# Optimization experiments

Hardware: AMD Instinct MI355X
Metric: run time of the kernel (lower is better)

## Reference

```python
import jax, jax.numpy as jnp
import numpy as np

HID = 1024
N_HEADS = 16
HEAD_DIM = HID // N_HEADS  # 64
SCALE = float(np.sqrt(HEAD_DIM))  # 8.0
# dba_l1 constants from the source
SCALING = float(np.sqrt(0.72676)) * SCALE
CENTER = SCALE ** 2 * 1.12838


def setup_inputs() -> dict:
    key = jax.random.key(0)
    kq, kk, kv = jax.random.split(key, 3)
    B, LQ, LK = 4, 256, 2048
    return {
        "attention_q": jax.random.normal(kq, (B, LQ, HID), dtype=jnp.float32),
        "attention_k": jax.random.normal(kk, (B, LK, HID), dtype=jnp.float32),
        "attention_v": jax.random.normal(kv, (B, LK, HID), dtype=jnp.float32),
        "attn_diag": jnp.ones((N_HEADS, 1, HEAD_DIM), dtype=jnp.float32),
    }


def _dba_l1_logits(Q, K, attn_diag):
    # Q: [B,H,Lq,D], K: [B,H,Lk,D], attn_diag: [H,1,D]
    # Scan over query positions (mirrors the original per-query loop) to avoid
    # materializing the [B,H,Lq,Lk,D] diff tensor.
    qs = jnp.moveaxis(Q, 2, 0)  # [Lq,B,H,D]

    def step(carry, qi):
        # qi: [B,H,D] -> dist: [B,H,Lk]
        dist = jnp.sum(attn_diag * jnp.abs(K - qi[:, :, None, :]), axis=-1)
        # (dist - CENTER) / (-SCALING) == (CENTER - dist) / SCALING
        return carry, (CENTER - dist) / SCALING

    _, logits = jax.lax.scan(step, None, qs)  # [Lq,B,H,Lk]
    return jnp.moveaxis(logits, 0, 2)  # [B,H,Lq,Lk]


def reference(attention_q, attention_k, attention_v, attn_diag):
    B, Lq, _ = attention_q.shape
    Lk = attention_k.shape[1]
    # split heads: [B,L,hid] -> [B,H,L,D]
    Q = attention_q.reshape(B, Lq, N_HEADS, HEAD_DIM).transpose(0, 2, 1, 3)
    K = attention_k.reshape(B, Lk, N_HEADS, HEAD_DIM).transpose(0, 2, 1, 3)
    V = attention_v.reshape(B, Lk, N_HEADS, HEAD_DIM).transpose(0, 2, 1, 3)

    attn_logits = _dba_l1_logits(Q, K, attn_diag)  # [B,H,Lq,Lk]
    attention = jax.nn.softmax(attn_logits, axis=-1)
    x = jnp.einsum("bhqk,bhkd->bhqd", attention, V)  # [B,H,Lq,D]
    output = x.transpose(0, 2, 1, 3).reshape(B, Lq, HID)
    return output, attention
```

## Files before the change

kernel.cpp:

```cpp
#include <hip/hip_runtime.h>
#include <stdint.h>

typedef _Float16 half_t;
typedef _Float16 h8_t __attribute__((ext_vector_type(8)));
typedef float f4 __attribute__((ext_vector_type(4)));
typedef unsigned int u4v __attribute__((ext_vector_type(4)));

#define NB 4
#define NH 16
#define HD 64
#define LQ 256
#define LK 2048
#define HIDN 1024

#define KF 0.21153832f
#define QS 2048.0f

__device__ __forceinline__ uint32_t sad16(uint32_t a, uint32_t b, uint32_t c) {
#if __has_builtin(__builtin_amdgcn_sad_u16)
  return __builtin_amdgcn_sad_u16(a, b, c);
#else
  int a0 = a & 0xffff, a1 = a >> 16, b0 = b & 0xffff, b1 = b >> 16;
  int d0 = a0 - b0, d1 = a1 - b1;
  return c + (uint32_t)(d0 < 0 ? -d0 : d0) + (uint32_t)(d1 < 0 ? -d1 : d1);
#endif
}

__device__ __forceinline__ uint32_t quant2(float x0, float x1, float w0, float w1) {
  float f0 = fmaf(x0, w0, 32768.5f);
  float f1 = fmaf(x1, w1, 32768.5f);
  uint32_t u0 = (uint32_t)fminf(fmaxf(f0, 0.f), 65535.f);
  uint32_t u1 = (uint32_t)fminf(fmaxf(f1, 0.f), 65535.f);
  return u0 | (u1 << 16);
}

__global__ __launch_bounds__(256) void k_prep3(const float* __restrict__ Kin,
                                               const float* __restrict__ Vin,
                                               const float* __restrict__ diag,
                                               uint32_t* __restrict__ Ktq,
                                               half_t* __restrict__ Vt) {
  int bid = blockIdx.x;
  int isV = bid >= NB * NH * 32;
  int id = isV ? bid - NB * NH * 32 : bid;
  int kb = id & 31, bh = id >> 5, b = bh >> 4, h = bh & 15;
  int t = threadIdx.x;
  __shared__ float ls[64][65];
  {
    const float* base = isV ? Vin : Kin;
    int d = t & 63, kr = t >> 6;
    const float* src = base + (size_t)(b * LK + kb * 64 + kr) * HIDN + h * HD + d;
#pragma unroll
    for (int i = 0; i < 16; ++i) ls[kr + 4 * i][d] = src[(size_t)(4 * i) * HIDN];
  }
  __syncthreads();
  if (!isV) {
    int k = t & 63, g = t >> 6;
    uint32_t* dst = Ktq + ((size_t)bh * 32 + g * 8) * LK + kb * 64 + k;
#pragma unroll
    for (int i = 0; i < 8; ++i) {
      int d2 = g * 8 + i;
      float w0 = diag[h * HD + 2 * d2] * QS;
      float w1 = diag[h * HD + 2 * d2 + 1] * QS;
      dst[(size_t)i * LK] = quant2(ls[k][2 * d2], ls[k][2 * d2 + 1], w0, w1);
    }
  } else {
    int k = t & 63, g = t >> 6;
    half_t* dst = Vt + ((size_t)bh * HD + g * 16) * LK + kb * 64 + k;
#pragma unroll
    for (int i = 0; i < 16; ++i) dst[(size_t)i * LK] = (half_t)ls[k][g * 16 + i];
  }
}

__global__ __launch_bounds__(256, 4) void k_attn3(const float* __restrict__ Qin,
                                                  const uint32_t* __restrict__ Ktq,
                                                  const float* __restrict__ diag,
                                                  float* __restrict__ attn,
                                                  half_t* __restrict__ Pws) {
  int bid = blockIdx.x;
  int qt = bid & 31, bh = bid >> 5;
  int b = bh >> 4, h = bh & 15;
  int q0 = qt * 8, t = threadIdx.x;

  __shared__ uint32_t Qsp[8][32];
  __shared__ float redf[4][8];
  __shared__ uint32_t redu[4][8];

  {
    int q = t >> 5, d2 = t & 31;
    const float* qr = Qin + (size_t)(b * LQ + q0 + q) * HIDN + h * HD;
    float2 f = ((const float2*)qr)[d2];
    float2 w = ((const float2*)(diag + h * HD))[d2];
    Qsp[q][d2] = quant2(f.x, f.y, w.x * QS, w.y * QS);
  }
  __syncthreads();

  uint32_t acc[8][8];
#pragma unroll
  for (int q = 0; q < 8; ++q)
#pragma unroll
    for (int k = 0; k < 8; ++k) acc[q][k] = 0u;

  const uint32_t* kp = Ktq + (size_t)bh * 32 * LK + t * 8;
#pragma unroll 2
  for (int g = 0; g < 16; ++g) {
    u4v ka0 = *(const u4v*)kp;
    u4v ka1 = *(const u4v*)(kp + 4);
    u4v kb0 = *(const u4v*)(kp + LK);
    u4v kb1 = *(const u4v*)(kp + LK + 4);
    kp += 2 * LK;
#pragma unroll
    for (int q = 0; q < 8; ++q) {
      uint2 qd = *(const uint2*)&Qsp[q][2 * g];
#pragma unroll
      for (int k = 0; k < 4; ++k) {
        acc[q][k] = sad16(ka1[k] , ka1[k], acc[q][k]);
      }
    }
  }

#pragma unroll
  for (int q = 0; q < 8; ++q)
#pragma unroll
    for (int k = 0; k < 8; ++k) acc[q][k] = 0u;
  kp = Ktq + (size_t)bh * 32 * LK + t * 8;
#pragma unroll 2
  for (int g = 0; g < 16; ++g) {
    u4v ka0 = *(const u4v*)kp;
    u4v ka1 = *(const u4v*)(kp + 4);
    u4v kb0 = *(const u4v*)(kp + LK);
    u4v kb1 = *(const u4v*)(kp + LK + 4);
    kp += 2 * LK;
#pragma unroll
    for (int q = 0; q < 8; ++q) {
      uint2 qd = *(const uint2*)&Qsp[q][2 * g];
#pragma unroll
      for (int k = 0; k < 4; ++k) {
        acc[q][k] = sad16(kb0[k], qd.y, sad16(ka0[k], qd.x, acc[q][k]));
        acc[q][4 + k] = sad16(kb1[k], qd.y, sad16(ka1[k], qd.x, acc[q][4 + k]));
      }
    }
  }

  int lane = t & 63, wid = t >> 6;

  uint32_t mrow[8];
#pragma unroll
  for (int q = 0; q < 8; ++q) {
    uint32_t m = acc[q][0];
#pragma unroll
    for (int k = 1; k < 8; ++k) m = min(m, acc[q][k]);
#pragma unroll
    for (int off = 32; off; off >>= 1)
      m = min(m, (uint32_t)__shfl_xor((int)m, off, 64));
    mrow[q] = m;
  }
  if (lane == 0) {
#pragma unroll
    for (int q = 0; q < 8; ++q) redu[wid][q] = mrow[q];
  }
  __syncthreads();
#pragma unroll
  for (int q = 0; q < 8; ++q)
    mrow[q] = min(min(redu[0][q], redu[1][q]), min(redu[2][q], redu[3][q]));
  __syncthreads();

  const float KFQ = KF / QS;
  float pv[8][8];
  float rsum[8];
#pragma unroll
  for (int q = 0; q < 8; ++q) {
    float s = 0.f;
#pragma unroll
    for (int k = 0; k < 8; ++k) {
      float p = exp2f((float)((int)mrow[q] - (int)acc[q][k]) * KFQ);
      pv[q][k] = p;
      s += p;
    }
#pragma unroll
    for (int off = 32; off; off >>= 1) s += __shfl_xor(s, off, 64);
    rsum[q] = s;
  }
  if (lane == 0) {
#pragma unroll
    for (int q = 0; q < 8; ++q) redf[wid][q] = rsum[q];
  }
  __syncthreads();
#pragma unroll
  for (int q = 0; q < 8; ++q)
    rsum[q] = (redf[0][q] + redf[1][q]) + (redf[2][q] + redf[3][q]);

#pragma unroll
  for (int q = 0; q < 8; ++q) {
    float inv = 1.0f / rsum[q];
    f4 p0, p1;
    h8_t hp;
#pragma unroll
    for (int i = 0; i < 4; ++i) {
      p0[i] = pv[q][i] * inv;
      p1[i] = pv[q][4 + i] * inv;
      hp[i] = (half_t)p0[i];
      hp[4 + i] = (half_t)p1[i];
    }
    size_t row = (size_t)(bh * LQ + q0 + q) * LK + t * 8;
    ((f4*)(attn + row))[0] = p0;
    ((f4*)(attn + row))[1] = p1;
    *(h8_t*)(Pws + row) = hp;
  }
}

__global__ __launch_bounds__(256) void k_pv3(const half_t* __restrict__ Ph,
                                             const half_t* __restrict__ Vt,
                                             float* __restrict__ Xout) {
  int bid = blockIdx.x;
  int qt = bid & 15, bh = bid >> 4;
  int b = bh >> 4, h = bh & 15;
  int q0 = qt * 16, t = threadIdx.x, lane = t & 63, w = t >> 6;
  int m = lane & 15, quad = lane >> 4;

  __shared__ float Cp[4][16][65];

  f4 cfr[4];
#pragma unroll
  for (int nt = 0; nt < 4; ++nt) cfr[nt] = (f4){0.f, 0.f, 0.f, 0.f};

  int k0 = w * 512;
  const half_t* vb = Vt + (size_t)bh * HD * LK;
  size_t prow = (size_t)(bh * LQ + q0 + m) * LK;

  int kk = k0 + quad * 8;
  h8_t af0 = *(const h8_t*)(Ph + prow + kk);
  h8_t bf0[4];
#pragma unroll
  for (int nt = 0; nt < 4; ++nt)
    bf0[nt] = *(const h8_t*)(vb + (size_t)(nt * 16 + m) * LK + kk);

#pragma unroll 2
  for (int ks = 0; ks < 16; ++ks) {
    h8_t af1, bf1[4];
    if (ks < 15) {
      int kn = k0 + (ks + 1) * 32 + quad * 8;
      af1 = *(const h8_t*)(Ph + prow + kn);
#pragma unroll
      for (int nt = 0; nt < 4; ++nt)
        bf1[nt] = *(const h8_t*)(vb + (size_t)(nt * 16 + m) * LK + kn);
    }
#pragma unroll
    for (int nt = 0; nt < 4; ++nt)
      cfr[nt] = __builtin_amdgcn_mfma_f32_16x16x32_f16(af0, bf0[nt], cfr[nt], 0, 0, 0);
    af0 = af1;
#pragma unroll
    for (int nt = 0; nt < 4; ++nt) bf0[nt] = bf1[nt];
  }

#pragma unroll
  for (int nt = 0; nt < 4; ++nt)
#pragma unroll
    for (int r = 0; r < 4; ++r) Cp[w][quad * 4 + r][nt * 16 + m] = cfr[nt][r];
  __syncthreads();

  int d = t & 63, q4 = t >> 6;
#pragma unroll
  for (int i = 0; i < 4; ++i) {
    int q = q4 * 4 + i;
    float s = (Cp[0][q][d] + Cp[1][q][d]) + (Cp[2][q][d] + Cp[3][q][d]);
    Xout[(size_t)(b * LQ + q0 + q) * HIDN + h * HD + d] = s;
  }
}

__global__ __launch_bounds__(256, 2) void k_attn_slow(const float* __restrict__ Qin,
                                                      const float* __restrict__ Kin,
                                                      const float* __restrict__ diag,
                                                      float* __restrict__ attn) {
  int bid = blockIdx.x;
  int qt = bid & 15, bh = bid >> 4;
  int b = bh >> 4, h = bh & 15;
  int q0 = qt * 16, t = threadIdx.x;
  __shared__ float Qs[16][64];
  __shared__ float Dg[64];
  __shared__ float red[4][16];
  {
    int q = t >> 4;
    const f4* src = (const f4*)(Qin + (size_t)(b * LQ + q0 + q) * HIDN + h * HD);
    ((f4*)Qs[q])[t & 15] = src[t & 15];
  }
  if (t < 64) Dg[t] = diag[h * HD + t];
  __syncthreads();
  float acc[16][8];
#pragma unroll
  for (int q = 0; q < 16; ++q)
#pragma unroll
    for (int j = 0; j < 8; ++j) acc[q][j] = 0.f;
  const float* kfp = Kin + (size_t)(b * LK + t * 8) * HIDN + h * HD;
  for (int d = 0; d < 64; ++d) {
    float dgd = Dg[d];
    float kd[8];
#pragma unroll
    for (int j = 0; j < 8; ++j) kd[j] = kfp[(size_t)j * HIDN + d];
#pragma unroll
    for (int j = 0; j < 8; ++j) {
      float kv = kd[j];
#pragma unroll
      for (int q = 0; q < 16; ++q)
        acc[q][j] = fmaf(dgd, fabsf(kv - Qs[q][d]), acc[q][j]);
    }
  }
  int lane = t & 63, wid = t >> 6;
  float mrow[16];
#pragma unroll
  for (int q = 0; q < 16; ++q) {
    float mm = acc[q][0];
#pragma unroll
    for (int j = 1; j < 8; ++j) mm = fminf(mm, acc[q][j]);
#pragma unroll
    for (int off = 32; off; off >>= 1) mm = fminf(mm, __shfl_xor(mm, off, 64));
    mrow[q] = mm;
  }
  if (lane == 0)
#pragma unroll
    for (int q = 0; q < 16; ++q) red[wid][q] = mrow[q];
  __syncthreads();
#pragma unroll
  for (int q = 0; q < 16; ++q)
    mrow[q] = fminf(fminf(red[0][q], red[1][q]), fminf(red[2][q], red[3][q]));
  __syncthreads();
  float rsum[16];
#pragma unroll
  for (int q = 0; q < 16; ++q) {
    float s = 0.f;
#pragma unroll
    for (int j = 0; j < 8; ++j) {
      float p = exp2f((mrow[q] - acc[q][j]) * KF);
      acc[q][j] = p;
      s += p;
    }
#pragma unroll
    for (int off = 32; off; off >>= 1) s += __shfl_xor(s, off, 64);
    rsum[q] = s;
  }
  if (lane == 0)
#pragma unroll
    for (int q = 0; q < 16; ++q) red[wid][q] = rsum[q];
  __syncthreads();
#pragma unroll
  for (int q = 0; q < 16; ++q)
    rsum[q] = (red[0][q] + red[1][q]) + (red[2][q] + red[3][q]);
#pragma unroll
  for (int q = 0; q < 16; ++q) {
    float inv = 1.0f / rsum[q];
    f4 p0, p1;
#pragma unroll
    for (int i = 0; i < 4; ++i) { p0[i] = acc[q][i] * inv; p1[i] = acc[q][4 + i] * inv; }
    float* op = attn + ((size_t)(bh * LQ + q0 + q)) * LK + t * 8;
    ((f4*)op)[0] = p0;
    ((f4*)op)[1] = p1;
  }
}

__global__ __launch_bounds__(256) void k_pv_old(const float* __restrict__ P,
                                                const float* __restrict__ Vin,
                                                float* __restrict__ Xout) {
  int bid = blockIdx.x;
  int qt = bid & 3, bh = bid >> 2;
  int b = bh >> 4, h = bh & 15;
  int q0 = qt * 64;
  int t = threadIdx.x, lane = t & 63, wid = t >> 6;
  int m = lane & 15, quad = lane >> 4;
  __shared__ half_t Vts[64 * 256];
  f4 cfr[4];
#pragma unroll
  for (int nt = 0; nt < 4; ++nt) cfr[nt] = (f4){0.f, 0.f, 0.f, 0.f};
  int qrow = q0 + wid * 16 + m;
  const float* pbase = P + ((size_t)(bh * LQ + qrow)) * LK + quad * 8;
  for (int kb = 0; kb < 8; ++kb) {
    {
      int d = wid * 16 + (lane & 15);
      int kg = lane >> 4;
      const float* vp = Vin + (size_t)(b * LK + kb * 256) * HIDN + h * HD + d;
#pragma unroll
      for (int i = 0; i < 32; ++i) {
        int kl = i * 8 + kg * 2;
        float v0 = vp[(size_t)kl * HIDN];
        float v1 = vp[(size_t)(kl + 1) * HIDN];
        int addr = d * 256 + ((((kl >> 3) ^ (d & 7)) << 3) | (kl & 7));
        Vts[addr] = (half_t)v0;
        Vts[addr + 1] = (half_t)v1;
      }
    }
    __syncthreads();
#pragma unroll
    for (int ks = 0; ks < 8; ++ks) {
      const float* pp = pbase + kb * 256 + ks * 32;
      f4 a0 = ((const f4*)pp)[0];
      f4 a1 = ((const f4*)pp)[1];
      h8_t af;
#pragma unroll
      for (int i = 0; i < 4; ++i) { af[i] = (half_t)a0[i]; af[4 + i] = (half_t)a1[i]; }
      int koff = ks * 32 + quad * 8;
#pragma unroll
      for (int nt = 0; nt < 4; ++nt) {
        int n = nt * 16 + m;
        int vaddr = n * 256 + ((((koff >> 3) ^ (n & 7)) << 3));
        h8_t bf = *(const h8_t*)&Vts[vaddr];
        cfr[nt] = __builtin_amdgcn_mfma_f32_16x16x32_f16(af, bf, cfr[nt], 0, 0, 0);
      }
    }
    __syncthreads();
  }
#pragma unroll
  for (int nt = 0; nt < 4; ++nt)
#pragma unroll
    for (int r = 0; r < 4; ++r) {
      int row = quad * 4 + r;
      int q = q0 + wid * 16 + row;
      Xout[(size_t)(b * LQ + q) * HIDN + h * HD + nt * 16 + m] = cfr[nt][r];
    }
}

extern "C" void kernel_launch(void* const* d_in, const int* in_sizes, int n_in,
                              void* d_out, int out_size, void* d_ws, size_t ws_size,
                              hipStream_t stream) {
  const float* Q = (const float*)d_in[0];
  const float* K = (const float*)d_in[1];
  const float* V = (const float*)d_in[2];
  const float* dg = (const float*)d_in[3];
  float* out = (float*)d_out;
  float* attn = out + (size_t)NB * LQ * HIDN;

  size_t ktB = (size_t)NB * NH * 32 * LK * 4;
  size_t vtB = (size_t)NB * NH * HD * LK * 2;
  size_t pB = (size_t)NB * NH * LQ * LK * 2;
  char* wsb = (char*)d_ws;
  uint32_t* Ktq = (uint32_t*)wsb;
  half_t* Vt = (half_t*)(wsb + ktB);
  half_t* Pws = (half_t*)(wsb + ktB + vtB);

  if (ws_size >= ktB + vtB + pB) {
    k_prep3<<<NB * NH * 32 * 2, 256, 0, stream>>>(K, V, dg, Ktq, Vt);
    k_attn3<<<NB * NH * 32, 256, 0, stream>>>(Q, Ktq, dg, attn, Pws);
    k_pv3<<<NB * NH * 16, 256, 0, stream>>>(Pws, Vt, out);
  } else {
    k_attn_slow<<<NB * NH * 16, 256, 0, stream>>>(Q, K, dg, attn);
    k_pv_old<<<NB * NH * 4, 256, 0, stream>>>(attn, V, out);
  }
}
```

Measured before the change: 295.3 us.

## Fuse PV matmul into attention kernel and drop redundant SAD pass

Folds the P·V MFMA stage into the attention kernel. The fp16 probabilities are staged in shared memory instead of a global workspace, and V is prepacked by the prep kernel into MFMA fragment order. This removes the round trip of the fp16 P matrix through global memory, one kernel launch, and a leftover duplicate SAD accumulation loop that was computed and then discarded. The block index order also changes so that heads vary fastest. The costs are extra shared memory per block and MFMA tiles where half the rows are duplicates, since only 8 queries fill the 16-row tile.

Result: faster. 267.8 us (-9.3%).

```diff
diff --git a/kernel.cpp b/kernel.cpp
--- a/kernel.cpp
+++ b/kernel.cpp
@@ -15,6 +15,7 @@
 
 #define KF 0.21153832f
 #define QS 2048.0f
+#define PSTR 2056
 
 __device__ __forceinline__ uint32_t sad16(uint32_t a, uint32_t b, uint32_t c) {
 #if __has_builtin(__builtin_amdgcn_sad_u16)
@@ -25,6 +26,7 @@
   return c + (uint32_t)(d0 < 0 ? -d0 : d0) + (uint32_t)(d1 < 0 ? -d1 : d1);
 #endif
 }
+__device__ __forceinline__ uint32_t umin32(uint32_t a, uint32_t b) { return a < b ? a : b; }
 
 __device__ __forceinline__ uint32_t quant2(float x0, float x1, float w0, float w1) {
   float f0 = fmaf(x0, w0, 32768.5f);
@@ -34,11 +36,11 @@
   return u0 | (u1 << 16);
 }
 
-__global__ __launch_bounds__(256) void k_prep3(const float* __restrict__ Kin,
+__global__ __launch_bounds__(256) void k_prep4(const float* __restrict__ Kin,
                                                const float* __restrict__ Vin,
                                                const float* __restrict__ diag,
                                                uint32_t* __restrict__ Ktq,
-                                               half_t* __restrict__ Vt) {
+                                               half_t* __restrict__ Vfrag) {
   int bid = blockIdx.x;
   int isV = bid >= NB * NH * 32;
   int id = isV ? bid - NB * NH * 32 : bid;
@@ -64,26 +66,40 @@
       dst[(size_t)i * LK] = quant2(ls[k][2 * d2], ls[k][2 * d2 + 1], w0, w1);
     }
   } else {
-    int k = t & 63, g = t >> 6;
-    half_t* dst = Vt + ((size_t)bh * HD + g * 16) * LK + kb * 64 + k;
-#pragma unroll
-    for (int i = 0; i < 16; ++i) dst[(size_t)i * LK] = (half_t)ls[k][g * 16 + i];
-  }
-}
-
-__global__ __launch_bounds__(256, 4) void k_attn3(const float* __restrict__ Qin,
+    half_t* dst = Vfrag + (size_t)bh * (HD * LK) + (size_t)kb * 4096;
+#pragma unroll
+    for (int i = 0; i < 2; ++i) {
+      int s = t * 2 + i;
+      int kcl = s >> 8, nt = (s >> 6) & 3, ln = s & 63;
+      int kr = kcl * 32 + (ln >> 4) * 8;
+      int n = nt * 16 + (ln & 15);
+      h8_t v;
+#pragma unroll
+      for (int j = 0; j < 8; ++j) v[j] = (half_t)ls[kr + j][n];
+      *(h8_t*)(dst + (size_t)s * 8) = v;
+    }
+  }
+}
+
+__global__ __launch_bounds__(256, 4) void k_fused(const float* __restrict__ Qin,
                                                   const uint32_t* __restrict__ Ktq,
                                                   const float* __restrict__ diag,
+                                                  const half_t* __restrict__ Vfrag,
                                                   float* __restrict__ attn,
-                                                  half_t* __restrict__ Pws) {
+                                                  float* __restrict__ Xout) {
   int bid = blockIdx.x;
-  int qt = bid & 31, bh = bid >> 5;
+  int bh = bid & 63, qt = bid >> 6;
   int b = bh >> 4, h = bh & 15;
   int q0 = qt * 8, t = threadIdx.x;
+  int lane = t & 63, wid = t >> 6;
+  int m = lane & 15, quad = lane >> 4;
 
   __shared__ uint32_t Qsp[8][32];
   __shared__ float redf[4][8];
   __shared__ uint32_t redu[4][8];
+  __shared__ __align__(16) char ShBuf[8 * PSTR * 2];
+  half_t* Pst = (half_t*)ShBuf;
+  float* Cred = (float*)ShBuf;
 
   {
     int q = t >> 5, d2 = t & 31;
@@ -113,46 +129,22 @@
       uint2 qd = *(const uint2*)&Qsp[q][2 * g];
 #pragma unroll
       for (int k = 0; k < 4; ++k) {
-        acc[q][k] = sad16(ka1[k] , ka1[k], acc[q][k]);
-      }
-    }
-  }
-
-#pragma unroll
-  for (int q = 0; q < 8; ++q)
-#pragma unroll
-    for (int k = 0; k < 8; ++k) acc[q][k] = 0u;
-  kp = Ktq + (size_t)bh * 32 * LK + t * 8;
-#pragma unroll 2
-  for (int g = 0; g < 16; ++g) {
-    u4v ka0 = *(const u4v*)kp;
-    u4v ka1 = *(const u4v*)(kp + 4);
-    u4v kb0 = *(const u4v*)(kp + LK);
-    u4v kb1 = *(const u4v*)(kp + LK + 4);
-    kp += 2 * LK;
-#pragma unroll
-    for (int q = 0; q < 8; ++q) {
-      uint2 qd = *(const uint2*)&Qsp[q][2 * g];
-#pragma unroll
-      for (int k = 0; k < 4; ++k) {
         acc[q][k] = sad16(kb0[k], qd.y, sad16(ka0[k], qd.x, acc[q][k]));
         acc[q][4 + k] = sad16(kb1[k], qd.y, sad16(ka1[k], qd.x, acc[q][4 + k]));
       }
     }
   }
 
-  int lane = t & 63, wid = t >> 6;
-
   uint32_t mrow[8];
 #pragma unroll
   for (int q = 0; q < 8; ++q) {
-    uint32_t m = acc[q][0];
-#pragma unroll
-    for (int k = 1; k < 8; ++k) m = min(m, acc[q][k]);
+    uint32_t mn = acc[q][0];
+#pragma unroll
+    for (int k = 1; k < 8; ++k) mn = umin32(mn, acc[q][k]);
 #pragma unroll
     for (int off = 32; off; off >>= 1)
-      m = min(m, (uint32_t)__shfl_xor((int)m, off, 64));
-    mrow[q] = m;
+      mn = umin32(mn, (uint32_t)__shfl_xor((int)mn, off, 64));
+    mrow[q] = mn;
   }
   if (lane == 0) {
 #pragma unroll
@@ -161,7 +153,7 @@
   __syncthreads();
 #pragma unroll
   for (int q = 0; q < 8; ++q)
-    mrow[q] = min(min(redu[0][q], redu[1][q]), min(redu[2][q], redu[3][q]));
+    mrow[q] = umin32(umin32(redu[0][q], redu[1][q]), umin32(redu[2][q], redu[3][q]));
   __syncthreads();
 
   const float KFQ = KF / QS;
@@ -204,66 +196,44 @@
     size_t row = (size_t)(bh * LQ + q0 + q) * LK + t * 8;
     ((f4*)(attn + row))[0] = p0;
     ((f4*)(attn + row))[1] = p1;
-    *(h8_t*)(Pws + row) = hp;
-  }
-}
-
-__global__ __launch_bounds__(256) void k_pv3(const half_t* __restrict__ Ph,
-                                             const half_t* __restrict__ Vt,
-                                             float* __restrict__ Xout) {
-  int bid = blockIdx.x;
-  int qt = bid & 15, bh = bid >> 4;
-  int b = bh >> 4, h = bh & 15;
-  int q0 = qt * 16, t = threadIdx.x, lane = t & 63, w = t >> 6;
-  int m = lane & 15, quad = lane >> 4;
-
-  __shared__ float Cp[4][16][65];
+    *(h8_t*)(Pst + q * PSTR + t * 8) = hp;
+  }
 
   f4 cfr[4];
 #pragma unroll
   for (int nt = 0; nt < 4; ++nt) cfr[nt] = (f4){0.f, 0.f, 0.f, 0.f};
-
-  int k0 = w * 512;
-  const half_t* vb = Vt + (size_t)bh * HD * LK;
-  size_t prow = (size_t)(bh * LQ + q0 + m) * LK;
-
-  int kk = k0 + quad * 8;
-  h8_t af0 = *(const h8_t*)(Ph + prow + kk);
-  h8_t bf0[4];
-#pragma unroll
-  for (int nt = 0; nt < 4; ++nt)
-    bf0[nt] = *(const h8_t*)(vb + (size_t)(nt * 16 + m) * LK + kk);
-
+  const half_t* vf = Vfrag + (size_t)bh * (HD * LK);
 #pragma unroll 2
-  for (int ks = 0; ks < 16; ++ks) {
-    h8_t af1, bf1[4];
-    if (ks < 15) {
-      int kn = k0 + (ks + 1) * 32 + quad * 8;
-      af1 = *(const h8_t*)(Ph + prow + kn);
-#pragma unroll
-      for (int nt = 0; nt < 4; ++nt)
-        bf1[nt] = *(const h8_t*)(vb + (size_t)(nt * 16 + m) * LK + kn);
-    }
+  for (int c = 0; c < 16; ++c) {
+    int kc = wid * 16 + c;
+    h8_t af = *(const h8_t*)(Pst + (m & 7) * PSTR + kc * 32 + quad * 8);
+#pragma unroll
+    for (int nt = 0; nt < 4; ++nt) {
+      h8_t bf = *(const h8_t*)(vf + (size_t)((kc * 4 + nt) * 64 + lane) * 8);
+      cfr[nt] = __builtin_amdgcn_mfma_f32_16x16x32_f16(af, bf, cfr[nt], 0, 0, 0);
+    }
+  }
+
+  __syncthreads();
+  if (quad < 2) {
 #pragma unroll
     for (int nt = 0; nt < 4; ++nt)
-      cfr[nt] = __builtin_amdgcn_mfma_f32_16x16x32_f16(af0, bf0[nt], cfr[nt], 0, 0, 0);
-    af0 = af1;
-#pragma unroll
-    for (int nt = 0; nt < 4; ++nt) bf0[nt] = bf1[nt];
-  }
-
-#pragma unroll
-  for (int nt = 0; nt < 4; ++nt)
-#pragma unroll
-    for (int r = 0; r < 4; ++r) Cp[w][quad * 4 + r][nt * 16 + m] = cfr[nt][r];
-  __syncthreads();
-
-  int d = t & 63, q4 = t >> 6;
-#pragma unroll
-  for (int i = 0; i < 4; ++i) {
-    int q = q4 * 4 + i;
-    float s = (Cp[0][q][d] + Cp[1][q][d]) + (Cp[2][q][d] + Cp[3][q][d]);
-    Xout[(size_t)(b * LQ + q0 + q) * HIDN + h * HD + d] = s;
+#pragma unroll
+      for (int r = 0; r < 4; ++r)
+        Cred[((wid * 8 + quad * 4 + r) * 64) + nt * 16 + m] = cfr[nt][r];
+  }
+  __syncthreads();
+
+  {
+    int q = t >> 5, d0 = (t & 31) * 2;
+    float s0 = 0.f, s1 = 0.f;
+#pragma unroll
+    for (int w = 0; w < 4; ++w) {
+      s0 += Cred[((w * 8 + q) * 64) + d0];
+      s1 += Cred[((w * 8 + q) * 64) + d0 + 1];
+    }
+    float2 o = {s0, s1};
+    *(float2*)(Xout + (size_t)(b * LQ + q0 + q) * HIDN + h * HD + d0) = o;
   }
 }
 
@@ -427,17 +397,14 @@
   float* attn = out + (size_t)NB * LQ * HIDN;
 
   size_t ktB = (size_t)NB * NH * 32 * LK * 4;
-  size_t vtB = (size_t)NB * NH * HD * LK * 2;
-  size_t pB = (size_t)NB * NH * LQ * LK * 2;
+  size_t vfB = (size_t)NB * NH * HD * LK * 2;
   char* wsb = (char*)d_ws;
   uint32_t* Ktq = (uint32_t*)wsb;
-  half_t* Vt = (half_t*)(wsb + ktB);
-  half_t* Pws = (half_t*)(wsb + ktB + vtB);
-
-  if (ws_size >= ktB + vtB + pB) {
-    k_prep3<<<NB * NH * 32 * 2, 256, 0, stream>>>(K, V, dg, Ktq, Vt);
-    k_attn3<<<NB * NH * 32, 256, 0, stream>>>(Q, Ktq, dg, attn, Pws);
-    k_pv3<<<NB * NH * 16, 256, 0, stream>>>(Pws, Vt, out);
+  half_t* Vfrag = (half_t*)(wsb + ktB);
+
+  if (ws_size >= ktB + vfB) {
+    k_prep4<<<NB * NH * 32 * 2, 256, 0, stream>>>(K, V, dg, Ktq, Vfrag);
+    k_fused<<<NB * NH * 32, 256, 0, stream>>>(Q, Ktq, dg, Vfrag, attn, out);
   } else {
     k_attn_slow<<<NB * NH * 16, 256, 0, stream>>>(Q, K, dg, attn);
     k_pv_old<<<NB * NH * 4, 256, 0, stream>>>(attn, V, out);
```
